# Kernel tuning notes

Measured on AMD Instinct MI355X. Metric: run time of the kernel, lower is better.

Reference implementation:

```python
import jax, jax.numpy as jnp
import numpy as np

B, H, W, C = 4, 64, 64, 256
CK = C // 8  # f/g projection dim = 32


def setup_inputs() -> dict:
    key = jax.random.key(0)
    ks = jax.random.split(key, 4)
    x = jax.random.normal(ks[0], (B, H, W, C), dtype=jnp.float32)
    Wf = jax.random.normal(ks[1], (C, CK), dtype=jnp.float32) * (1.0 / np.sqrt(C))
    Wg = jax.random.normal(ks[2], (C, CK), dtype=jnp.float32) * (1.0 / np.sqrt(C))
    Wh = jax.random.normal(ks[3], (C, C), dtype=jnp.float32) * (1.0 / np.sqrt(C))
    bf = jnp.zeros((CK,), jnp.float32)
    bg = jnp.zeros((CK,), jnp.float32)
    bh = jnp.zeros((C,), jnp.float32)
    return {"x": x, "Wf": Wf, "bf": bf, "Wg": Wg, "bg": bg, "Wh": Wh, "bh": bh}


def reference(x, Wf, bf, Wg, bg, Wh, bh):
    b, h, w, c = x.shape
    n = h * w
    xf = x.reshape(b, n, c)  # 1x1 conv == per-pixel matmul
    f = xf @ Wf + bf         # [b, n, c/8]  (keys)
    g = xf @ Wg + bg         # [b, n, c/8]  (queries)
    hh = xf @ Wh + bh        # [b, n, c]    (values)
    # s[i,j] = g_i . f_j  (tf.matmul(g, f, transpose_b=True))
    s = jnp.einsum('bik,bjk->bij', g, f)
    beta = jax.nn.softmax(s, axis=-1)
    o = jnp.einsum('bij,bjc->bic', beta, hh)
    return x + o.reshape(b, h, w, c)
```

## Files before the change

### kernel.cpp

```cpp
#include <hip/hip_runtime.h>
#include <math.h>

#define CDIM 256
#define CKD  32
#define NPIX 4096
#define BATCH 4
#define NMACRO (NPIX / 64)

typedef __attribute__((ext_vector_type(8)))  short bf16x8;
typedef __attribute__((ext_vector_type(16))) float f32x16;

__device__ inline ushort f2bf(float x) {
    unsigned u = __float_as_uint(x);
    u += 0x7fffu + ((u >> 16) & 1u);
    return (ushort)(u >> 16);
}
__device__ inline unsigned packbf(float a, float b) {
    return (unsigned)f2bf(a) | ((unsigned)f2bf(b) << 16);
}

#define LDS_ASYNC16(gptr, lptr) \
  __builtin_amdgcn_global_load_lds((const __attribute__((address_space(1))) void*)(gptr), \
                                   (__attribute__((address_space(3))) void*)(lptr), 16, 0, 0)

__global__ __launch_bounds__(256) void prep_kernel(
    const float* __restrict__ Wh, const float* __restrict__ Wf,
    const float* __restrict__ Wg, ushort* __restrict__ Wt)
{
    const int k = blockIdx.x;
    const int c = threadIdx.x;
    Wt[c * 256 + k] = f2bf(Wh[k * 256 + c]);
    if (c < 32)
        Wt[(256 + c) * 256 + k] = f2bf(Wf[k * CKD + c]);
    else if (c < 64)
        Wt[(288 + (c - 32)) * 256 + k] = f2bf(Wg[k * CKD + (c - 32)]);
}

__global__ __launch_bounds__(256) void proj_kernel(
    const float*  __restrict__ x,
    const ushort* __restrict__ Wt,
    const float*  __restrict__ bfp, const float* __restrict__ bgp,
    const float*  __restrict__ bhp,
    ushort* __restrict__ fo,
    ushort* __restrict__ go,
    ushort* __restrict__ glo,
    ushort* __restrict__ ht)
{
    __shared__ ushort wls[2][1280 * 8];
    __shared__ ushort xls[2][128 * 8];

    const int tid  = threadIdx.x;
    const int w    = tid >> 6;
    const int lane = tid & 63;
    const int hl   = lane >> 5;
    const int ln   = lane & 31;
    const int bid  = blockIdx.x;
    const long long px0 = (long long)bid * 32;
    const int b    = (int)(px0 >> 12);
    const int n0   = (int)(px0 & (NPIX - 1));
    const int kt   = n0 >> 6;
    const int koff = n0 & 63;

    const int sx_px = tid & 31, sx_jq = tid >> 5;

    #pragma unroll
    for (int i = 0; i < 5; ++i) {
        int s = i * 256 + tid;
        int n = s >> 2, o = ((s & 3) - (n >> 1)) & 3;
        LDS_ASYNC16(Wt + n * 256 + o * 8, &wls[0][s * 8]);
    }
    {
        float4 v = *(const float4*)(x + (px0 + sx_px) * CDIM + sx_jq * 4);
        uint2 p; p.x = packbf(v.x, v.y); p.y = packbf(v.z, v.w);
        *(uint2*)&xls[0][((sx_jq >> 1) * 32 + sx_px) * 8 + (sx_jq & 1) * 4] = p;
    }

    f32x16 acc0={0,0,0,0,0,0,0,0,0,0,0,0,0,0,0,0};
    f32x16 acc1={0,0,0,0,0,0,0,0,0,0,0,0,0,0,0,0};
    f32x16 accfg={0,0,0,0,0,0,0,0,0,0,0,0,0,0,0,0};

    for (int sl = 0; sl < 8; ++sl) {
        const int cur = sl & 1;
        __syncthreads();
        if (sl + 1 < 8) {
            const int nxt = cur ^ 1;
            #pragma unroll
            for (int i = 0; i < 5; ++i) {
                int s = i * 256 + tid;
                int n = s >> 2, o = ((s & 3) - (n >> 1)) & 3;
                LDS_ASYNC16(Wt + n * 256 + (sl + 1) * 32 + o * 8, &wls[nxt][s * 8]);
            }
            float4 v = *(const float4*)(x + (px0 + sx_px) * CDIM + (sl + 1) * 32 + sx_jq * 4);
            uint2 p; p.x = packbf(v.x, v.y); p.y = packbf(v.z, v.w);
            *(uint2*)&xls[nxt][((sx_jq >> 1) * 32 + sx_px) * 8 + (sx_jq & 1) * 4] = p;
        }

        #pragma unroll
        for (int st = 0; st < 2; ++st) {
            const int o = st * 2 + hl;
            #define LDW(n) (*(const bf16x8*)&wls[cur][((n) * 4 + (((o) + ((n) >> 1)) & 3)) * 8])
            bf16x8 xb  = *(const bf16x8*)&xls[cur][(o * 32 + ln) * 8];
            bf16x8 wa0 = LDW(w * 64 + ln);
            bf16x8 wa1 = LDW(w * 64 + 32 + ln);
            acc0 = __builtin_amdgcn_mfma_f32_32x32x16_bf16(wa0, xb, acc0, 0, 0, 0);
            acc1 = __builtin_amdgcn_mfma_f32_32x32x16_bf16(wa1, xb, acc1, 0, 0, 0);
            if (w < 2) {
                bf16x8 wfg = LDW(256 + w * 32 + ln);
                accfg = __builtin_amdgcn_mfma_f32_32x32x16_bf16(xb, wfg, accfg, 0, 0, 0);
            }
            #undef LDW
        }
    }

    ushort* htt = ht + ((long long)(b * 64 + kt) * CDIM) * 64 + koff;
    #pragma unroll
    for (int r = 0; r < 16; ++r) {
        const int rowD = (r & 3) + 8 * (r >> 2) + 4 * hl;
        int c0 = w * 64 + rowD, c1 = c0 + 32;
        htt[(long long)c0 * 64 + ln] = f2bf(acc0[r] + bhp[c0]);
        htt[(long long)c1 * 64 + ln] = f2bf(acc1[r] + bhp[c1]);
    }
    if (w < 2) {
        const float bb = (w ? bgp : bfp)[ln];
        #pragma unroll
        for (int r = 0; r < 16; ++r) {
            const int rowD = (r & 3) + 8 * (r >> 2) + 4 * hl;
            float v = accfg[r] + bb;
            ushort hi = f2bf(v);
            long long idx = (px0 + rowD) * CKD + ln;
            if (w == 0) {
                fo[idx] = hi;
            } else {
                go[idx] = hi;
                float hif = __uint_as_float(((unsigned)hi) << 16);
                glo[idx] = f2bf(v - hif);
            }
        }
    }
}

__global__ __launch_bounds__(256) void attn_kernel(
    const float*  __restrict__ x,
    const ushort* __restrict__ fk,
    const ushort* __restrict__ gq,
    const ushort* __restrict__ glo,
    const ushort* __restrict__ hv,
    float* __restrict__ out)
{
    __shared__ ushort hh_lds[2][1024 * 8];
    __shared__ ushort f_lds[2][256 * 8];
    __shared__ ushort p_lds[512 * 8];
    __shared__ float  l_red[2][64];

    const int tid  = threadIdx.x;
    const int w    = tid >> 6;
    const int lane = tid & 63;
    const int hl   = lane >> 5;
    const int ln   = lane & 31;

    const int bid = blockIdx.x;
    const int chs = bid & 1;
    const int b   = (bid >> 1) & 3;
    const int qt  = bid >> 3;
    const int q0  = qt * 64;

    const int qb = w & 1;
    const int kh = w >> 1;

    const long long bbase = (long long)b * NPIX;
    const ushort* fbase = fk + bbase * CKD;
    const ushort* htb   = hv + (long long)b * 64 * (CDIM * 64);

    const ushort* gp  = gq  + (bbase + q0 + qb * 32 + ln) * CKD;
    const ushort* glp = glo + (bbase + q0 + qb * 32 + ln) * CKD;
    const bf16x8 ga0 = *(const bf16x8*)(gp + hl * 8);
    const bf16x8 ga1 = *(const bf16x8*)(gp + 16 + hl * 8);
    const bf16x8 gl0 = *(const bf16x8*)(glp + hl * 8);
    const bf16x8 gl1 = *(const bf16x8*)(glp + 16 + hl * 8);

    #pragma unroll
    for (int i = 0; i < 4; ++i) {
        int s = i * 256 + tid;
        int c = s >> 3, j = ((s & 7) - c) & 7;
        LDS_ASYNC16(htb + (long long)(chs * 128 + c) * 64 + j * 8, &hh_lds[0][s * 8]);
    }
    LDS_ASYNC16(fbase + (long long)(tid & 63) * CKD + (tid >> 6) * 8, &f_lds[0][tid * 8]);

    f32x16 accA={0,0,0,0,0,0,0,0,0,0,0,0,0,0,0,0};
    f32x16 accB={0,0,0,0,0,0,0,0,0,0,0,0,0,0,0,0};
    float lsum = 0.f;

    for (int kt = 0; kt < NMACRO; ++kt) {
        const int cur = kt & 1;
        __syncthreads();

        f32x16 S={0,0,0,0,0,0,0,0,0,0,0,0,0,0,0,0};
        {
            bf16x8 fb0 = *(const bf16x8*)&f_lds[cur][((hl)     * 64 + kh * 32 + ln) * 8];
            bf16x8 fb1 = *(const bf16x8*)&f_lds[cur][((2 + hl) * 64 + kh * 32 + ln) * 8];
            S = __builtin_amdgcn_mfma_f32_32x32x16_bf16(fb0, ga0, S, 0, 0, 0);
            S = __builtin_amdgcn_mfma_f32_32x32x16_bf16(fb0, gl0, S, 0, 0, 0);
            S = __builtin_amdgcn_mfma_f32_32x32x16_bf16(fb1, ga1, S, 0, 0, 0);
            S = __builtin_amdgcn_mfma_f32_32x32x16_bf16(fb1, gl1, S, 0, 0, 0);
        }

        {
            float p[16];
            #pragma unroll
            for (int r = 0; r < 16; ++r) {
                p[r] = __expf(fminf(S[r], 80.f));
                lsum += p[r];
            }
            const int q = qb * 32 + ln;
            #pragma unroll
            for (int m = 0; m < 4; ++m) {
                uint2 d;
                d.x = packbf(p[4 * m + 0], p[4 * m + 1]);
                d.y = packbf(p[4 * m + 2], p[4 * m + 3]);
                int oct = kh * 4 + m;
                int slot = q * 8 + ((oct + q) & 7);
                *(uint2*)&p_lds[slot * 8 + hl * 4] = d;
            }
        }
        __syncthreads();

        if (kt + 1 < NMACRO) {
            const int nxt = cur ^ 1;
            const long long tb = (long long)(kt + 1) * (CDIM * 64);
            #pragma unroll
            for (int i = 0; i < 4; ++i) {
                int s = i * 256 + tid;
                int c = s >> 3, j = ((s & 7) - c) & 7;
                LDS_ASYNC16(htb + tb + (long long)(chs * 128 + c) * 64 + j * 8,
                            &hh_lds[nxt][s * 8]);
            }
            LDS_ASYNC16(fbase + (long long)((kt + 1) * 64 + (tid & 63)) * CKD + (tid >> 6) * 8,
                        &f_lds[nxt][tid * 8]);
        }

        const int qa = qb * 32 + ln;
        const int ca = kh * 64 + ln, cb2 = kh * 64 + 32 + ln;
        #pragma unroll
        for (int ch = 0; ch < 4; ++ch) {
            const int oct = ch * 2 + hl;
            bf16x8 pa = *(const bf16x8*)&p_lds[(qa * 8 + ((oct + qa) & 7)) * 8];
            bf16x8 h0 = *(const bf16x8*)&hh_lds[cur][(ca  * 8 + ((oct + ca)  & 7)) * 8];
            bf16x8 h1 = *(const bf16x8*)&hh_lds[cur][(cb2 * 8 + ((oct + cb2) & 7)) * 8];
            accA = __builtin_amdgcn_mfma_f32_32x32x16_bf16(pa, h0, accA, 0, 0, 0);
            accB = __builtin_amdgcn_mfma_f32_32x32x16_bf16(pa, h1, accB, 0, 0, 0);
        }
    }

    lsum += __shfl_xor(lsum, 32);
    if (hl == 0) l_red[kh][qb * 32 + ln] = lsum;
    __syncthreads();

    #pragma unroll
    for (int r = 0; r < 16; ++r) {
        const int rowD = (r & 3) + 8 * (r >> 2) + 4 * hl;
        const int ql = qb * 32 + rowD;
        float linv = 1.f / (l_red[0][ql] + l_red[1][ql]);
        long long rg = (bbase + q0 + ql) * CDIM + chs * 128 + kh * 64 + ln;
        out[rg]      = x[rg]      + accA[r] * linv;
        out[rg + 32] = x[rg + 32] + accB[r] * linv;
    }
}

extern "C" void kernel_launch(void* const* d_in, const int* in_sizes, int n_in,
                              void* d_out, int out_size, void* d_ws, size_t ws_size,
                              hipStream_t stream) {
    const float* x  = (const float*)d_in[0];
    const float* Wf = (const float*)d_in[1];
    const float* bf = (const float*)d_in[2];
    const float* Wg = (const float*)d_in[3];
    const float* bg = (const float*)d_in[4];
    const float* Wh = (const float*)d_in[5];
    const float* bh = (const float*)d_in[6];
    float* out = (float*)d_out;

    ushort* fbf = (ushort*)d_ws;
    ushort* gbf = fbf + BATCH * NPIX * CKD;
    ushort* glo = gbf + BATCH * NPIX * CKD;
    ushort* ht  = glo + BATCH * NPIX * CKD;
    ushort* Wt  = ht + BATCH * NPIX * CDIM;

    prep_kernel<<<dim3(256), 256, 0, stream>>>(Wh, Wf, Wg, Wt);
    proj_kernel<<<dim3(512), 256, 0, stream>>>(x, Wt, bf, bg, bh, fbf, gbf, glo, ht);
    attn_kernel<<<dim3(512), 256, 0, stream>>>(x, fbf, gbf, glo, ht, out);
}
```

Measured before the change: 173.5 us.

## Keep softmax probabilities in registers and split keys across waves in attention

In the attention kernel the P tile no longer goes through LDS. Each wave builds its own MFMA A-operand from registers using a cross-half lane shuffle, computes all 128 channels for its key half, and the two key halves are reduced through LDS at the end. This removes a __syncthreads and the LDS round trip per key tile, and issues the next-tile prefetch earlier. It also raises occupancy hints with launch_bounds(256,2), swizzles the x staging layout in proj to avoid LDS bank conflicts, and rewrites the weight transpose prep as a tiled LDS transpose. The cost is twice the accumulator registers and the same hh loads now read by both qb waves.

```diff
diff --git a/kernel.cpp b/kernel.cpp
--- a/kernel.cpp
+++ b/kernel.cpp
@@ -27,13 +27,44 @@
     const float* __restrict__ Wh, const float* __restrict__ Wf,
     const float* __restrict__ Wg, ushort* __restrict__ Wt)
 {
-    const int k = blockIdx.x;
-    const int c = threadIdx.x;
-    Wt[c * 256 + k] = f2bf(Wh[k * 256 + c]);
-    if (c < 32)
-        Wt[(256 + c) * 256 + k] = f2bf(Wf[k * CKD + c]);
-    else if (c < 64)
-        Wt[(288 + (c - 32)) * 256 + k] = f2bf(Wg[k * CKD + (c - 32)]);
+    __shared__ float ls[64 * 65];
+    const int tid = threadIdx.x;
+    const int bid = blockIdx.x;
+
+    if (bid < 16) {
+        const int k0 = (bid & 3) * 64, c0 = (bid >> 2) * 64;
+        #pragma unroll
+        for (int i = 0; i < 16; ++i) {
+            int r = i * 4 + (tid >> 6), c = tid & 63;
+            ls[r * 65 + c] = Wh[(k0 + r) * 256 + c0 + c];
+        }
+        __syncthreads();
+        #pragma unroll
+        for (int i = 0; i < 16; ++i) {
+            int cr = i * 4 + (tid >> 6), k = tid & 63;
+            Wt[(c0 + cr) * 256 + k0 + k] = f2bf(ls[k * 65 + cr]);
+        }
+    } else {
+        const float* W = (bid == 16) ? Wf : Wg;
+        const int rbase = 256 + (bid - 16) * 32;
+        #pragma unroll
+        for (int kh2 = 0; kh2 < 2; ++kh2) {
+            __syncthreads();
+            #pragma unroll
+            for (int i = 0; i < 16; ++i) {
+                int flat = i * 256 + tid;
+                int k = flat >> 5, c = flat & 31;
+                ls[c * 129 + k] = W[(kh2 * 128 + k) * 32 + c];
+            }
+            __syncthreads();
+            #pragma unroll
+            for (int i = 0; i < 16; ++i) {
+                int flat = i * 256 + tid;
+                int c = flat >> 7, k = flat & 127;
+                Wt[(rbase + c) * 256 + kh2 * 128 + k] = f2bf(ls[c * 129 + k]);
+            }
+        }
+    }
 }
 
 __global__ __launch_bounds__(256) void proj_kernel(
@@ -61,7 +92,9 @@
     const int kt   = n0 >> 6;
     const int koff = n0 & 63;
 
-    const int sx_px = tid & 31, sx_jq = tid >> 5;
+    const int sx_px = tid >> 3, sx_j = tid & 7;
+    const int sx_o = sx_j >> 1, sx_h = sx_j & 1;
+    const int sx_slot = sx_o * 32 + ((sx_px + 2 * sx_o) & 31);
 
     #pragma unroll
     for (int i = 0; i < 5; ++i) {
@@ -70,9 +103,9 @@
         LDS_ASYNC16(Wt + n * 256 + o * 8, &wls[0][s * 8]);
     }
     {
-        float4 v = *(const float4*)(x + (px0 + sx_px) * CDIM + sx_jq * 4);
+        float4 v = *(const float4*)(x + (px0 + sx_px) * CDIM + sx_j * 4);
         uint2 p; p.x = packbf(v.x, v.y); p.y = packbf(v.z, v.w);
-        *(uint2*)&xls[0][((sx_jq >> 1) * 32 + sx_px) * 8 + (sx_jq & 1) * 4] = p;
+        *(uint2*)&xls[0][sx_slot * 8 + sx_h * 4] = p;
     }
 
     f32x16 acc0={0,0,0,0,0,0,0,0,0,0,0,0,0,0,0,0};
@@ -90,16 +123,16 @@
                 int n = s >> 2, o = ((s & 3) - (n >> 1)) & 3;
                 LDS_ASYNC16(Wt + n * 256 + (sl + 1) * 32 + o * 8, &wls[nxt][s * 8]);
             }
-            float4 v = *(const float4*)(x + (px0 + sx_px) * CDIM + (sl + 1) * 32 + sx_jq * 4);
+            float4 v = *(const float4*)(x + (px0 + sx_px) * CDIM + (sl + 1) * 32 + sx_j * 4);
             uint2 p; p.x = packbf(v.x, v.y); p.y = packbf(v.z, v.w);
-            *(uint2*)&xls[nxt][((sx_jq >> 1) * 32 + sx_px) * 8 + (sx_jq & 1) * 4] = p;
+            *(uint2*)&xls[nxt][sx_slot * 8 + sx_h * 4] = p;
         }
 
         #pragma unroll
         for (int st = 0; st < 2; ++st) {
             const int o = st * 2 + hl;
             #define LDW(n) (*(const bf16x8*)&wls[cur][((n) * 4 + (((o) + ((n) >> 1)) & 3)) * 8])
-            bf16x8 xb  = *(const bf16x8*)&xls[cur][(o * 32 + ln) * 8];
+            bf16x8 xb  = *(const bf16x8*)&xls[cur][(o * 32 + ((ln + 2 * o) & 31)) * 8];
             bf16x8 wa0 = LDW(w * 64 + ln);
             bf16x8 wa1 = LDW(w * 64 + 32 + ln);
             acc0 = __builtin_amdgcn_mfma_f32_32x32x16_bf16(wa0, xb, acc0, 0, 0, 0);
@@ -139,7 +172,7 @@
     }
 }
 
-__global__ __launch_bounds__(256) void attn_kernel(
+__global__ __launch_bounds__(256, 2) void attn_kernel(
     const float*  __restrict__ x,
     const ushort* __restrict__ fk,
     const ushort* __restrict__ gq,
@@ -149,7 +182,6 @@
 {
     __shared__ ushort hh_lds[2][1024 * 8];
     __shared__ ushort f_lds[2][256 * 8];
-    __shared__ ushort p_lds[512 * 8];
     __shared__ float  l_red[2][64];
 
     const int tid  = threadIdx.x;
@@ -186,13 +218,29 @@
     }
     LDS_ASYNC16(fbase + (long long)(tid & 63) * CKD + (tid >> 6) * 8, &f_lds[0][tid * 8]);
 
-    f32x16 accA={0,0,0,0,0,0,0,0,0,0,0,0,0,0,0,0};
-    f32x16 accB={0,0,0,0,0,0,0,0,0,0,0,0,0,0,0,0};
+    f32x16 acc[4];
+    #pragma unroll
+    for (int t = 0; t < 4; ++t)
+        acc[t] = (f32x16){0,0,0,0,0,0,0,0,0,0,0,0,0,0,0,0};
     float lsum = 0.f;
 
     for (int kt = 0; kt < NMACRO; ++kt) {
         const int cur = kt & 1;
         __syncthreads();
+
+        if (kt + 1 < NMACRO) {
+            const int nxt = cur ^ 1;
+            const long long tb = (long long)(kt + 1) * (CDIM * 64);
+            #pragma unroll
+            for (int i = 0; i < 4; ++i) {
+                int s = i * 256 + tid;
+                int c = s >> 3, j = ((s & 7) - c) & 7;
+                LDS_ASYNC16(htb + tb + (long long)(chs * 128 + c) * 64 + j * 8,
+                            &hh_lds[nxt][s * 8]);
+            }
+            LDS_ASYNC16(fbase + (long long)((kt + 1) * 64 + (tid & 63)) * CKD + (tid >> 6) * 8,
+                        &f_lds[nxt][tid * 8]);
+        }
 
         f32x16 S={0,0,0,0,0,0,0,0,0,0,0,0,0,0,0,0};
         {
@@ -204,65 +252,71 @@
             S = __builtin_amdgcn_mfma_f32_32x32x16_bf16(fb1, gl1, S, 0, 0, 0);
         }
 
-        {
-            float p[16];
+        float p[16];
+        #pragma unroll
+        for (int r = 0; r < 16; ++r) {
+            p[r] = __expf(fminf(S[r], 80.f));
+            lsum += p[r];
+        }
+        unsigned U[8];
+        #pragma unroll
+        for (int m = 0; m < 8; ++m) U[m] = packbf(p[2*m], p[2*m+1]);
+
+        #pragma unroll
+        for (int ck = 0; ck < 2; ++ck) {
+            unsigned vx = hl ? U[4*ck]     : U[4*ck + 2];
+            unsigned vy = hl ? U[4*ck + 1] : U[4*ck + 3];
+            unsigned rx = (unsigned)__shfl_xor((int)vx, 32);
+            unsigned ry = (unsigned)__shfl_xor((int)vy, 32);
+            union { unsigned i[4]; bf16x8 v; } pf;
+            pf.i[0] = hl ? rx : U[4*ck];
+            pf.i[1] = hl ? ry : U[4*ck + 1];
+            pf.i[2] = hl ? U[4*ck + 2] : rx;
+            pf.i[3] = hl ? U[4*ck + 3] : ry;
+            bf16x8 pa = pf.v;
+            #pragma unroll
+            for (int ct = 0; ct < 4; ++ct) {
+                const int c = ct * 32 + ln;
+                const int oct = kh * 4 + ck * 2 + hl;
+                bf16x8 hb = *(const bf16x8*)&hh_lds[cur][(c * 8 + ((oct + c) & 7)) * 8];
+                acc[ct] = __builtin_amdgcn_mfma_f32_32x32x16_bf16(pa, hb, acc[ct], 0, 0, 0);
+            }
+        }
+    }
+
+    lsum += __shfl_xor(lsum, 32);
+    __syncthreads();
+    if (hl == 0) l_red[kh][qb * 32 + ln] = lsum;
+    float* O_s = (float*)hh_lds;
+    {
+        const int wct0 = kh ? 0 : 2;
+        #pragma unroll
+        for (int t = 0; t < 2; ++t) {
+            const int ct = wct0 + t;
             #pragma unroll
             for (int r = 0; r < 16; ++r) {
-                p[r] = __expf(fminf(S[r], 80.f));
-                lsum += p[r];
-            }
-            const int q = qb * 32 + ln;
-            #pragma unroll
-            for (int m = 0; m < 4; ++m) {
-                uint2 d;
-                d.x = packbf(p[4 * m + 0], p[4 * m + 1]);
-                d.y = packbf(p[4 * m + 2], p[4 * m + 3]);
-                int oct = kh * 4 + m;
-                int slot = q * 8 + ((oct + q) & 7);
-                *(uint2*)&p_lds[slot * 8 + hl * 4] = d;
-            }
-        }
-        __syncthreads();
-
-        if (kt + 1 < NMACRO) {
-            const int nxt = cur ^ 1;
-            const long long tb = (long long)(kt + 1) * (CDIM * 64);
-            #pragma unroll
-            for (int i = 0; i < 4; ++i) {
-                int s = i * 256 + tid;
-                int c = s >> 3, j = ((s & 7) - c) & 7;
-                LDS_ASYNC16(htb + tb + (long long)(chs * 128 + c) * 64 + j * 8,
-                            &hh_lds[nxt][s * 8]);
-            }
-            LDS_ASYNC16(fbase + (long long)((kt + 1) * 64 + (tid & 63)) * CKD + (tid >> 6) * 8,
-                        &f_lds[nxt][tid * 8]);
-        }
-
-        const int qa = qb * 32 + ln;
-        const int ca = kh * 64 + ln, cb2 = kh * 64 + 32 + ln;
-        #pragma unroll
-        for (int ch = 0; ch < 4; ++ch) {
-            const int oct = ch * 2 + hl;
-            bf16x8 pa = *(const bf16x8*)&p_lds[(qa * 8 + ((oct + qa) & 7)) * 8];
-            bf16x8 h0 = *(const bf16x8*)&hh_lds[cur][(ca  * 8 + ((oct + ca)  & 7)) * 8];
-            bf16x8 h1 = *(const bf16x8*)&hh_lds[cur][(cb2 * 8 + ((oct + cb2) & 7)) * 8];
-            accA = __builtin_amdgcn_mfma_f32_32x32x16_bf16(pa, h0, accA, 0, 0, 0);
-            accB = __builtin_amdgcn_mfma_f32_32x32x16_bf16(pa, h1, accB, 0, 0, 0);
-        }
-    }
-
-    lsum += __shfl_xor(lsum, 32);
-    if (hl == 0) l_red[kh][qb * 32 + ln] = lsum;
+                int rowD = (r & 3) + 8 * (r >> 2) + 4 * hl;
+                O_s[((qb * 4 + ct) * 32 + rowD) * 32 + ln] = acc[ct][r];
+            }
+        }
+    }
     __syncthreads();
 
-    #pragma unroll
-    for (int r = 0; r < 16; ++r) {
-        const int rowD = (r & 3) + 8 * (r >> 2) + 4 * hl;
-        const int ql = qb * 32 + rowD;
-        float linv = 1.f / (l_red[0][ql] + l_red[1][ql]);
-        long long rg = (bbase + q0 + ql) * CDIM + chs * 128 + kh * 64 + ln;
-        out[rg]      = x[rg]      + accA[r] * linv;
-        out[rg + 32] = x[rg + 32] + accB[r] * linv;
+    {
+        const int oct0 = kh ? 2 : 0;
+        #pragma unroll
+        for (int t = 0; t < 2; ++t) {
+            const int ct = oct0 + t;
+            #pragma unroll
+            for (int r = 0; r < 16; ++r) {
+                int rowD = (r & 3) + 8 * (r >> 2) + 4 * hl;
+                int ql = qb * 32 + rowD;
+                float linv = 1.f / (l_red[0][ql] + l_red[1][ql]);
+                float o = acc[ct][r] + O_s[((qb * 4 + ct) * 32 + rowD) * 32 + ln];
+                long long rg = (bbase + q0 + ql) * CDIM + chs * 128 + ct * 32 + ln;
+                out[rg] = x[rg] + o * linv;
+            }
+        }
     }
 }
 
@@ -284,7 +338,7 @@
     ushort* ht  = glo + BATCH * NPIX * CKD;
     ushort* Wt  = ht + BATCH * NPIX * CDIM;
 
-    prep_kernel<<<dim3(256), 256, 0, stream>>>(Wh, Wf, Wg, Wt);
+    prep_kernel<<<dim3(18), 256, 0, stream>>>(Wh, Wf, Wg, Wt);
     proj_kernel<<<dim3(512), 256, 0, stream>>>(x, Wt, bf, bg, bh, fbf, gbf, glo, ht);
     attn_kernel<<<dim3(512), 256, 0, stream>>>(x, fbf, gbf, glo, ht, out);
 }
```

Result: slower. 381.2 us (+119.8%).
